# Kernel tuning notes

Measured on AMD Instinct MI355X. Metric: run time of the kernel, lower is better.

## Reference

```python
import jax, jax.numpy as jnp
import numpy as np

DN = ('NCHW', 'OIHW', 'NCHW')

def conv(x, w, b, stride, pad):
    y = jax.lax.conv_general_dilated(x, w, (stride, stride), [(pad, pad), (pad, pad)], dimension_numbers=DN)
    return y if b is None else y + b[None, :, None, None]

def convT(x, w, b, stride, pad):
    # torch ConvTranspose2d weight layout: (in, out, kh, kw)
    wt = jnp.flip(w, (2, 3)).transpose(1, 0, 2, 3)
    p = w.shape[2] - 1 - pad
    y = jax.lax.conv_general_dilated(x, wt, (1, 1), [(p, p), (p, p)], lhs_dilation=(stride, stride), dimension_numbers=DN)
    return y + b[None, :, None, None]

def resblock(x, wa, wb):
    h = conv(jax.nn.relu(x), wa, None, 1, 1)   # 3x3, 128->32, no bias
    h = conv(jax.nn.relu(h), wb, None, 1, 0)   # 1x1, 32->128, no bias
    return x + h

def setup_inputs() -> dict:
    key = jax.random.key(0)
    ks = jax.random.split(key, 32)
    def w(i, shape):
        fan_in = int(np.prod(shape[1:]))
        return jax.random.normal(ks[i], shape, jnp.float32) * (1.0 / np.sqrt(fan_in))
    K, D = 512, 64
    inp = {
        'x':   jax.random.normal(ks[0], (16, 1, 256, 256), jnp.float32),
        'ew1': w(1, (64, 1, 4, 4)),    'eb1': jnp.zeros((64,), jnp.float32),
        'ew2': w(2, (128, 64, 4, 4)),  'eb2': jnp.zeros((128,), jnp.float32),
        'ew3': w(3, (128, 128, 3, 3)), 'eb3': jnp.zeros((128,), jnp.float32),
        'er1a': w(4, (32, 128, 3, 3)), 'er1b': w(5, (128, 32, 1, 1)),
        'er2a': w(6, (32, 128, 3, 3)), 'er2b': w(7, (128, 32, 1, 1)),
        'pw': w(8, (64, 128, 1, 1)),   'pb': jnp.zeros((64,), jnp.float32),
        'codebook': jax.random.uniform(ks[9], (K, D), jnp.float32, -1.0 / K, 1.0 / K),
        'dw1': w(10, (128, 64, 3, 3)), 'db1': jnp.zeros((128,), jnp.float32),
        'dr1a': w(11, (32, 128, 3, 3)), 'dr1b': w(12, (128, 32, 1, 1)),
        'dr2a': w(13, (32, 128, 3, 3)), 'dr2b': w(14, (128, 32, 1, 1)),
        'dtw1': w(15, (128, 64, 4, 4)), 'dtb1': jnp.zeros((64,), jnp.float32),  # ConvT: (in,out,kh,kw)
        'dtw2': w(16, (64, 1, 4, 4)),   'dtb2': jnp.zeros((1,), jnp.float32),
    }
    return inp

def vq(z, codebook, beta=0.25):
    zn = z.transpose(0, 2, 3, 1)                 # NHWC
    flat = zn.reshape(-1, codebook.shape[1])     # [N, D]
    d = jnp.sum(flat * flat, axis=1, keepdims=True) + jnp.sum(codebook * codebook, axis=1) - 2.0 * (flat @ codebook.T)  # [N, K]
    idx = jnp.argmin(d, axis=1)
    enc = jax.nn.one_hot(idx, codebook.shape[0], dtype=z.dtype)  # [N, K]
    q = codebook[idx].reshape(zn.shape)
    e_loss = jnp.mean(jnp.square(jax.lax.stop_gradient(q) - zn))
    q_loss = jnp.mean(jnp.square(q - jax.lax.stop_gradient(zn)))
    loss = q_loss + beta * e_loss
    q_st = zn + jax.lax.stop_gradient(q - zn)    # straight-through
    avg = jnp.mean(enc, axis=0)
    perplexity = jnp.exp(-jnp.sum(avg * jnp.log(avg + 1e-10)))
    return loss, q_st.transpose(0, 3, 1, 2), perplexity, enc

def reference(x, ew1, eb1, ew2, eb2, ew3, eb3, er1a, er1b, er2a, er2b, pw, pb, codebook, dw1, db1, dr1a, dr1b, dr2a, dr2b, dtw1, dtb1, dtw2, dtb2):
    # encoder
    h = jax.nn.relu(conv(x, ew1, eb1, 2, 1))
    h = jax.nn.relu(conv(h, ew2, eb2, 2, 1))
    h = conv(h, ew3, eb3, 1, 1)
    h = resblock(h, er1a, er1b)
    h = resblock(h, er2a, er2b)
    h = jax.nn.relu(h)
    z = conv(h, pw, pb, 1, 0)
    # vector quantizer
    loss, quantized, perplexity, encodings = vq(z, codebook)
    # decoder
    d = conv(quantized, dw1, db1, 1, 1)
    d = resblock(d, dr1a, dr1b)
    d = resblock(d, dr2a, dr2b)
    d = jax.nn.relu(convT(d, dtw1, dtb1, 2, 1))
    x_rec = convT(d, dtw2, dtb2, 2, 1)
    return (loss, x_rec, perplexity, encodings, quantized)
```

## Files before the change

kernel.cpp:

```cpp
#include <hip/hip_runtime.h>

#define TPB 256

typedef __attribute__((ext_vector_type(8))) short s8v;
typedef __attribute__((ext_vector_type(4))) float f4v;
typedef __bf16 bf16x8v __attribute__((ext_vector_type(8)));

__device__ inline short f2b(float f) {
    unsigned u = __builtin_bit_cast(unsigned, f);
    unsigned r = (u + 0x7FFF + ((u >> 16) & 1)) >> 16;
    return (short)r;
}
__device__ inline float b2f(short s) {
    unsigned u = ((unsigned)(unsigned short)s) << 16;
    return __builtin_bit_cast(float, u);
}
__device__ inline f4v mfma16(s8v a, s8v b, f4v c) {
    return __builtin_amdgcn_mfma_f32_16x16x32_bf16(
        __builtin_bit_cast(bf16x8v, a), __builtin_bit_cast(bf16x8v, b), c, 0, 0, 0);
}

struct WtDesc { const float* src; int CO, CI, T, iohw, start; };
struct WtArgs { WtDesc d[13]; int total; };

__global__ __launch_bounds__(256)
void prep_k(WtArgs a, short* dst, const float* __restrict__ cb,
            short* __restrict__ cbh, short* __restrict__ cbl, float* __restrict__ cbsq)
{
    const int bx = blockIdx.x;
    const int tid = threadIdx.x;
    if (bx >= 2560) {
        int c = (bx - 2560) * 256 + tid;
        const float* src = cb + (size_t)c * 64;
        const int nt = c >> 4, rl = c & 15;
        float sq = 0.f;
        for (int d = 0; d < 64; ++d) {
            float v = src[d];
            sq += v * v;
            short h = f2b(v);
            short lo = f2b(v - b2f(h));
            int kc = d >> 5, qd = (d >> 3) & 3, j = d & 7;
            int pos = ((kc * 32 + nt) << 9) + ((qd * 16 + rl) << 3) + j;
            cbh[pos] = h;
            cbl[pos] = lo;
        }
        cbsq[c] = sq;
        return;
    }
    int i = bx * 256 + tid;
    if (i >= a.total) return;
    int s = 0;
    for (int j = 1; j < 13; ++j) if (i >= a.d[j].start) s = j;
    int off = i - a.d[s].start;
    int CI = a.d[s].CI, CO = a.d[s].CO, T = a.d[s].T;
    int KC = CI >> 5, NT = CO >> 4;
    int j    = off & 7;
    int lane = (off >> 3) & 63;
    int rl = lane & 15, qd = lane >> 4;
    int blk = off >> 9;
    int nt  = blk % NT;
    int rest = blk / NT;
    int kc  = rest % KC;
    int tap = rest / KC;
    int co = nt * 16 + rl;
    int ci = kc * 32 + qd * 8 + j;
    float v = a.d[s].iohw ? a.d[s].src[(ci * CO + co) * T + tap]
                          : a.d[s].src[(co * CI + ci) * T + tap];
    dst[i] = f2b(v);
}

__global__ __launch_bounds__(256)
void conv1_k(const float* __restrict__ x, const float* __restrict__ w,
             const float* __restrict__ bias, short* __restrict__ out)
{
    __shared__ float sx[4 * 256];
    const int tid = threadIdx.x;
    const int bx = blockIdx.x;
    const int oh = ((bx & 7) << 4) | (bx >> 3);
    const int n = blockIdx.y;
    const int co = tid & 63, wv = tid >> 6;

    float wr[16];
#pragma unroll
    for (int t = 0; t < 16; ++t) wr[t] = w[co * 16 + t];
    const float b = bias[co];

    const float* xp = x + (size_t)n * 65536;
    for (int e = tid; e < 1024; e += 256) {
        int kh = e >> 8, col = e & 255;
        int ih = oh * 2 - 1 + kh;
        sx[e] = ((unsigned)ih < 256u) ? xp[ih * 256 + col] : 0.f;
    }
    __syncthreads();

    short* op = out + (((size_t)n * 128 + oh) * 128) * 64 + co;
#pragma unroll 4
    for (int i = 0; i < 32; ++i) {
        int ow = wv * 32 + i;
        int iwb = ow * 2 - 1;
        float acc = b;
#pragma unroll
        for (int kh = 0; kh < 4; ++kh) {
#pragma unroll
            for (int kw = 0; kw < 4; ++kw) {
                int iw = iwb + kw;
                float v = ((unsigned)iw < 256u) ? sx[kh * 256 + iw] : 0.f;
                acc = fmaf(v, wr[kh * 4 + kw], acc);
            }
        }
        op[(size_t)ow * 64] = f2b(fmaxf(acc, 0.f));
    }
}

template<int CI, int CO, bool RELU_IN, bool RELU_OUT, bool OUT_F32>
__global__ __launch_bounds__(256)
void pconv3s_k(const short* __restrict__ in, const short* __restrict__ wt,
               const float* __restrict__ bias, void* __restrict__ outv)
{
    constexpr int KC = CI / 32, NT = CO / 16;
    constexpr int NT2 = NT / 2;
    __shared__ short sA[3 * 66 * 40];

    const int tid = threadIdx.x;
    const int bx = blockIdx.x;
    const int oh = ((bx & 7) << 3) | (bx >> 3);
    const int n  = blockIdx.y;
    const short* inb = in + (size_t)n * 4096 * CI;
    const int w = tid >> 6, l = tid & 63, rl = l & 15, qd = l >> 4;
    const int mh = w & 1, nh = w >> 1;

    f4v acc[2][NT2];
#pragma unroll
    for (int a2 = 0; a2 < 2; ++a2)
#pragma unroll
        for (int nt = 0; nt < NT2; ++nt) acc[a2][nt] = (f4v)0.f;

    for (int kc = 0; kc < KC; ++kc) {
        __syncthreads();
        for (int e = tid; e < 792; e += 256) {
            int cell = e >> 2, kcn = e & 3;
            int hr = cell / 66, col = cell - hr * 66;
            int ih = oh - 1 + hr, iw = col - 1;
            s8v v = (s8v)0;
            if ((unsigned)ih < 64u && (unsigned)iw < 64u) {
                v = *(const s8v*)(inb + ((size_t)ih * 64 + iw) * CI + kc * 32 + kcn * 8);
                if (RELU_IN) {
#pragma unroll
                    for (int j = 0; j < 8; ++j) if (v[j] < (short)0) v[j] = 0;
                }
            }
            *(s8v*)&sA[(hr * 66 + col) * 40 + kcn * 8] = v;
        }
        __syncthreads();

#pragma unroll
        for (int tap = 0; tap < 9; ++tap) {
            const int kh = tap / 3, kw = tap % 3;
            s8v af[2];
#pragma unroll
            for (int a2 = 0; a2 < 2; ++a2)
                af[a2] = *(const s8v*)&sA[(kh * 66 + mh * 32 + a2 * 16 + rl + kw) * 40 + qd * 8];
            const short* wb = wt + (((size_t)(tap * KC + kc) * NT + nh * NT2) << 9) + l * 8;
#pragma unroll
            for (int nt = 0; nt < NT2; ++nt) {
                s8v b = *(const s8v*)(wb + ((size_t)nt << 9));
#pragma unroll
                for (int a2 = 0; a2 < 2; ++a2)
                    acc[a2][nt] = mfma16(af[a2], b, acc[a2][nt]);
            }
        }
    }

#pragma unroll
    for (int a2 = 0; a2 < 2; ++a2) {
#pragma unroll
        for (int rg = 0; rg < 4; ++rg) {
            int ow = mh * 32 + a2 * 16 + qd * 4 + rg;
            size_t row = (size_t)n * 4096 + (size_t)oh * 64 + ow;
#pragma unroll
            for (int nt = 0; nt < NT2; ++nt) {
                int co = nh * NT2 * 16 + nt * 16 + rl;
                float v = acc[a2][nt][rg];
                if (bias) v += bias[co];
                if (RELU_OUT) v = fmaxf(v, 0.f);
                if (OUT_F32) ((float*)outv)[row * CO + co] = v;
                else         ((short*)outv)[row * CO + co] = f2b(v);
            }
        }
    }
}

template<int Z>
__global__ __launch_bounds__(256)
void rfuse_k(const short* __restrict__ in, const short* __restrict__ wa,
             const short* __restrict__ wb, short* __restrict__ out,
             const short* __restrict__ wz, const float* __restrict__ zb,
             float* __restrict__ zout)
{
    __shared__ short smem[8704];
    short* sA = smem;
    short* sMid = smem;
    short* sZ = smem;

    const int tid = threadIdx.x;
    const int bx = blockIdx.x;
    const int oh = ((bx & 7) << 3) | (bx >> 3);
    const int n  = blockIdx.y;
    const short* inb = in + (size_t)n * 4096 * 128;
    const int w = tid >> 6, l = tid & 63, rl = l & 15, qd = l >> 4;

    f4v acc1[2];
    acc1[0] = (f4v)0.f; acc1[1] = (f4v)0.f;

    for (int kc = 0; kc < 4; ++kc) {
        __syncthreads();
        for (int e = tid; e < 792; e += 256) {
            int cell = e >> 2, kcn = e & 3;
            int hr = cell / 66, col = cell - hr * 66;
            int ih = oh - 1 + hr, iw = col - 1;
            s8v v = (s8v)0;
            if ((unsigned)ih < 64u && (unsigned)iw < 64u) {
                v = *(const s8v*)(inb + ((size_t)ih * 64 + iw) * 128 + kc * 32 + kcn * 8);
#pragma unroll
                for (int j = 0; j < 8; ++j) if (v[j] < (short)0) v[j] = 0;
            }
            *(s8v*)&sA[(hr * 66 + col) * 40 + kcn * 8] = v;
        }
        __syncthreads();

#pragma unroll
        for (int tap = 0; tap < 9; ++tap) {
            const int kh = tap / 3, kw = tap % 3;
            s8v af = *(const s8v*)&sA[(kh * 66 + w * 16 + rl + kw) * 40 + qd * 8];
            const short* wp = wa + (((size_t)(tap * 4 + kc) * 2) << 9) + l * 8;
            acc1[0] = mfma16(af, *(const s8v*)(wp),       acc1[0]);
            acc1[1] = mfma16(af, *(const s8v*)(wp + 512), acc1[1]);
        }
    }

    __syncthreads();
#pragma unroll
    for (int nt = 0; nt < 2; ++nt)
#pragma unroll
        for (int rg = 0; rg < 4; ++rg) {
            int m  = w * 16 + qd * 4 + rg;
            int co = nt * 16 + rl;
            sMid[m * 40 + co] = f2b(fmaxf(acc1[nt][rg], 0.f));
        }
    __syncthreads();

    f4v acc2[8];
#pragma unroll
    for (int nt = 0; nt < 8; ++nt) acc2[nt] = (f4v)0.f;

    s8v am = *(const s8v*)&sMid[(w * 16 + rl) * 40 + qd * 8];
#pragma unroll
    for (int nt = 0; nt < 8; ++nt) {
        s8v b = *(const s8v*)(wb + ((size_t)nt << 9) + l * 8);
        acc2[nt] = mfma16(am, b, acc2[nt]);
    }

    const size_t sp0 = (size_t)oh * 64;
    if (Z == 0) {
        short* outb = out + (size_t)n * 4096 * 128;
#pragma unroll
        for (int rg = 0; rg < 4; ++rg) {
            int m = w * 16 + qd * 4 + rg;
            size_t sp = sp0 + m;
#pragma unroll
            for (int nt = 0; nt < 8; ++nt) {
                int co = nt * 16 + rl;
                float v = acc2[nt][rg] + b2f(inb[sp * 128 + co]);
                outb[sp * 128 + co] = f2b(v);
            }
        }
    } else {
        __syncthreads();
#pragma unroll
        for (int rg = 0; rg < 4; ++rg) {
            int m = w * 16 + qd * 4 + rg;
            size_t sp = sp0 + m;
#pragma unroll
            for (int nt = 0; nt < 8; ++nt) {
                int co = nt * 16 + rl;
                float v = acc2[nt][rg] + b2f(inb[sp * 128 + co]);
                sZ[m * 136 + co] = f2b(fmaxf(v, 0.f));
            }
        }
        __syncthreads();

        f4v acc3[4];
#pragma unroll
        for (int nt = 0; nt < 4; ++nt) acc3[nt] = (f4v)0.f;
        s8v am2[4];
#pragma unroll
        for (int kc = 0; kc < 4; ++kc)
            am2[kc] = *(const s8v*)&sZ[(w * 16 + rl) * 136 + kc * 32 + qd * 8];
#pragma unroll
        for (int kc = 0; kc < 4; ++kc)
#pragma unroll
            for (int nt = 0; nt < 4; ++nt) {
                s8v b = *(const s8v*)(wz + (((size_t)(kc * 4 + nt)) << 9) + l * 8);
                acc3[nt] = mfma16(am2[kc], b, acc3[nt]);
            }
        const size_t zr0 = (size_t)n * 4096 + (size_t)oh * 64;
#pragma unroll
        for (int rg = 0; rg < 4; ++rg) {
            size_t row = zr0 + w * 16 + qd * 4 + rg;
#pragma unroll
            for (int nt = 0; nt < 4; ++nt) {
                int co = nt * 16 + rl;
                zout[row * 64 + co] = acc3[nt][rg] + zb[co];
            }
        }
    }
}

__global__ __launch_bounds__(256)
void pconv2_k(const short* __restrict__ in, const short* __restrict__ wt,
              const float* __restrict__ bias, short* __restrict__ out)
{
    __shared__ short sA[2 * 4 * 66 * 40];
    const int tid = threadIdx.x;
    const int bx = blockIdx.x;
    const int oh = ((bx & 7) << 3) | (bx >> 3);
    const int n = blockIdx.y;
    const short* inb = in + (size_t)n * 16384 * 64;
    const int w = tid >> 6, l = tid & 63, rl = l & 15, qd = l >> 4;
    const int mh = w & 1, nh = w >> 1;

    f4v acc[2][4];
#pragma unroll
    for (int a2 = 0; a2 < 2; ++a2)
#pragma unroll
        for (int nt = 0; nt < 4; ++nt) acc[a2][nt] = (f4v)0.f;

    for (int kc = 0; kc < 2; ++kc) {
        __syncthreads();
        for (int e = tid; e < 2112; e += 256) {
            int cell = e >> 2, kcn = e & 3;
            int par = cell / 264;
            int rem = cell - par * 264;
            int hr = rem / 66, c = rem - hr * 66;
            int iw = par ? (2 * c - 1) : (2 * c);
            int ih = oh * 2 - 1 + hr;
            s8v v = (s8v)0;
            if ((unsigned)ih < 128u && (unsigned)iw < 128u)
                v = *(const s8v*)(inb + ((size_t)ih * 128 + iw) * 64 + kc * 32 + kcn * 8);
            *(s8v*)&sA[((par * 4 + hr) * 66 + c) * 40 + kcn * 8] = v;
        }
        __syncthreads();

#pragma unroll
        for (int tap = 0; tap < 16; ++tap) {
            const int kh = tap >> 2, kw = tap & 3;
            const int par = 1 - (kw & 1), cofs = kw >> 1;
            s8v af[2];
#pragma unroll
            for (int a2 = 0; a2 < 2; ++a2) {
                int ow = mh * 32 + a2 * 16 + rl;
                af[a2] = *(const s8v*)&sA[((par * 4 + kh) * 66 + ow + cofs) * 40 + qd * 8];
            }
            const short* wb = wt + (((size_t)(tap * 2 + kc) * 8 + nh * 4) << 9) + l * 8;
#pragma unroll
            for (int nt = 0; nt < 4; ++nt) {
                s8v b = *(const s8v*)(wb + ((size_t)nt << 9));
#pragma unroll
                for (int a2 = 0; a2 < 2; ++a2)
                    acc[a2][nt] = mfma16(af[a2], b, acc[a2][nt]);
            }
        }
    }

#pragma unroll
    for (int a2 = 0; a2 < 2; ++a2) {
#pragma unroll
        for (int rg = 0; rg < 4; ++rg) {
            int ow = mh * 32 + a2 * 16 + qd * 4 + rg;
            size_t row = (size_t)n * 4096 + (size_t)oh * 64 + ow;
#pragma unroll
            for (int nt = 0; nt < 4; ++nt) {
                int co = nh * 64 + nt * 16 + rl;
                float v = acc[a2][nt][rg] + bias[co];
                out[row * 128 + co] = f2b(fmaxf(v, 0.f));
            }
        }
    }
}

__global__ __launch_bounds__(256)
void pct1_k(const short* __restrict__ in, const short* __restrict__ wt,
            const float* __restrict__ bias, short* __restrict__ out)
{
    __shared__ short sA[3 * 66 * 40];
    const int tid = threadIdx.x;
    const int bx = blockIdx.x, n = blockIdx.y;
    const int k8 = bx & 7;
    const int P  = (bx >> 3) & 1;
    const int q2 = k8 * 8 + (bx >> 4);
    const int oh0 = (q2 >> 1) * 4 + (q2 & 1);
    const int p = (oh0 + 1) & 1;
    const int ihb0 = (oh0 + 1 - p) >> 1;
    const short* inb = in + (size_t)n * 4096 * 128;
    const int w = tid >> 6, l = tid & 63, rl = l & 15, qd = l >> 4;
    const int mh = w & 1, nh = w >> 1;

    f4v acc[4][2];
#pragma unroll
    for (int a4 = 0; a4 < 4; ++a4)
#pragma unroll
        for (int nt = 0; nt < 2; ++nt) acc[a4][nt] = (f4v)0.f;

    for (int kc = 0; kc < 4; ++kc) {
        __syncthreads();
        for (int e = tid; e < 792; e += 256) {
            int cell = e >> 2, kcn = e & 3;
            int hr = cell / 66, c = cell - hr * 66;
            int ih = ihb0 - 1 + hr, iw = c - 1;
            s8v v = (s8v)0;
            if ((unsigned)ih < 64u && (unsigned)iw < 64u)
                v = *(const s8v*)(inb + ((size_t)ih * 64 + iw) * 128 + kc * 32 + kcn * 8);
            *(s8v*)&sA[(hr * 66 + c) * 40 + kcn * 8] = v;
        }
        __syncthreads();

#pragma unroll
        for (int a = 0; a < 2; ++a)
#pragma unroll
        for (int b = 0; b < 2; ++b) {
            const int kh = p + 2 * a;
            const int kw = (1 - P) + 2 * b;
            const int tap = kh * 4 + kw;
            const int hrw = mh + 1 - a;
            s8v af[4];
#pragma unroll
            for (int a4 = 0; a4 < 4; ++a4)
                af[a4] = *(const s8v*)&sA[(hrw * 66 + a4 * 16 + rl + P - b + 1) * 40 + qd * 8];
            const short* wbp = wt + (((size_t)(tap * 4 + kc) * 4 + nh * 2) << 9) + l * 8;
#pragma unroll
            for (int nt = 0; nt < 2; ++nt) {
                s8v bb = *(const s8v*)(wbp + ((size_t)nt << 9));
#pragma unroll
                for (int a4 = 0; a4 < 4; ++a4)
                    acc[a4][nt] = mfma16(af[a4], bb, acc[a4][nt]);
            }
        }
    }

#pragma unroll
    for (int a4 = 0; a4 < 4; ++a4) {
#pragma unroll
        for (int rg = 0; rg < 4; ++rg) {
            int j = a4 * 16 + qd * 4 + rg;
            int oh = oh0 + 2 * mh, ow = 2 * j + P;
            size_t pb = (((size_t)n * 128 + oh) * 128 + ow) * 64;
#pragma unroll
            for (int nt = 0; nt < 2; ++nt) {
                int co = nh * 32 + nt * 16 + rl;
                float v = acc[a4][nt][rg] + bias[co];
                out[pb + co] = f2b(fmaxf(v, 0.f));
            }
        }
    }
}

__global__ __launch_bounds__(256)
void convt2_k(const short* __restrict__ in, const float* __restrict__ w,
              const float* __restrict__ bias, float* __restrict__ out)
{
    __shared__ float sw[16 * 64];
    const int tid = threadIdx.x;
    for (int e = tid; e < 1024; e += 256) { int ci = e >> 4, tap = e & 15; sw[tap * 64 + ci] = w[e]; }
    __syncthreads();

    const int i = blockIdx.x * 256 + tid;
    const int n = i >> 16, s = i & 65535;
    const int oh = s >> 8, ow = s & 255;

    const int p = (oh + 1) & 1, q = (ow + 1) & 1;
    const int ihb = (oh + 1 - p) >> 1, iwb = (ow + 1 - q) >> 1;

    float acc = bias[0];
#pragma unroll
    for (int a = 0; a < 2; ++a) {
        int ih = ihb - a, kh = p + 2 * a;
        bool vr = (unsigned)ih < 128u;
#pragma unroll
        for (int b = 0; b < 2; ++b) {
            int iw = iwb - b, kw = q + 2 * b;
            if (vr && (unsigned)iw < 128u) {
                const short* ip = in + (((size_t)n * 128 + ih) * 128 + iw) * 64;
                const float* wp = &sw[(kh * 4 + kw) * 64];
#pragma unroll
                for (int c = 0; c < 64; c += 8) {
                    s8v v = *(const s8v*)(ip + c);
#pragma unroll
                    for (int j = 0; j < 8; ++j) acc += b2f(v[j]) * wp[c + j];
                }
            }
        }
    }
    out[i] = acc;
}

__global__ __launch_bounds__(256)
void vqm_k(const float* __restrict__ z, const short* __restrict__ cbh,
           const short* __restrict__ cbl, const float* __restrict__ cbsq,
           const float* __restrict__ cb,
           float* __restrict__ quant, short* __restrict__ qb,
           int* __restrict__ idxp, float* __restrict__ errbuf)
{
    __shared__ float zs[64 * 68];
    __shared__ short scb[2][8192];
    __shared__ int sidx[64];
    __shared__ float serr[4];
    float* qc = (float*)&scb[0][0];

    const int tid = threadIdx.x;
    const int w = tid >> 6, l = tid & 63, rl = l & 15, qd = l >> 4;
    const int r0 = blockIdx.x * 64;

    for (int e = tid; e < 1024; e += 256) {
        int row = e >> 4, c4 = e & 15;
        float4 t = ((const float4*)(z + (size_t)(r0 + row) * 64))[c4];
        *(float4*)&zs[row * 68 + c4 * 4] = t;
    }
    __syncthreads();

    s8v zh[2], zl[2];
#pragma unroll
    for (int kc = 0; kc < 2; ++kc) {
        const float* zp = &zs[(w * 16 + rl) * 68 + kc * 32 + qd * 8];
        s8v hi, lo;
#pragma unroll
        for (int j = 0; j < 8; ++j) {
            float v = zp[j];
            short h = f2b(v);
            hi[j] = h;
            lo[j] = f2b(v - b2f(h));
        }
        zh[kc] = hi; zl[kc] = lo;
    }

    float best[4]; int bidx[4];
#pragma unroll
    for (int rg = 0; rg < 4; ++rg) { best[rg] = 3.4e38f; bidx[rg] = 0; }

    for (int ch = 0; ch < 4; ++ch) {
        __syncthreads();
        for (int e = tid; e < 1024; e += 256) {
            int kcL = e >> 9, rest = e & 511;
            int ntl = rest >> 6, off = rest & 63;
            int srcIdx = (kcL * 32 + ch * 8 + ntl) * 64 + off;
            *(s8v*)&scb[0][e * 8] = ((const s8v*)cbh)[srcIdx];
            *(s8v*)&scb[1][e * 8] = ((const s8v*)cbl)[srcIdx];
        }
        __syncthreads();

        float sq[8];
#pragma unroll
        for (int nt = 0; nt < 8; ++nt) sq[nt] = cbsq[ch * 128 + nt * 16 + rl];

        f4v acc[8];
#pragma unroll
        for (int nt = 0; nt < 8; ++nt) acc[nt] = (f4v)0.f;
#pragma unroll
        for (int kc = 0; kc < 2; ++kc) {
#pragma unroll
            for (int nt = 0; nt < 8; ++nt) {
                s8v bh = *(const s8v*)&scb[0][(kc * 8 + nt) * 512 + l * 8];
                s8v bl = *(const s8v*)&scb[1][(kc * 8 + nt) * 512 + l * 8];
                acc[nt] = mfma16(zh[kc], bh, acc[nt]);
                acc[nt] = mfma16(zh[kc], bl, acc[nt]);
                acc[nt] = mfma16(zl[kc], bh, acc[nt]);
            }
        }

#pragma unroll
        for (int rg = 0; rg < 4; ++rg) {
            float bd = best[rg]; int bi = bidx[rg];
#pragma unroll
            for (int nt = 0; nt < 8; ++nt) {
                float d = sq[nt] - 2.f * acc[nt][rg];
                int code = ch * 128 + nt * 16 + rl;
                if (d < bd) { bd = d; bi = code; }
            }
            best[rg] = bd; bidx[rg] = bi;
        }
    }

#pragma unroll
    for (int rg = 0; rg < 4; ++rg) {
        float bd = best[rg]; int bi = bidx[rg];
#pragma unroll
        for (int off = 1; off < 16; off <<= 1) {
            float od = __shfl_xor(bd, off, 64);
            int   oi = __shfl_xor(bi, off, 64);
            if (od < bd || (od == bd && oi < bi)) { bd = od; bi = oi; }
        }
        if (rl == 0) sidx[w * 16 + qd * 4 + rg] = bi;
    }
    __syncthreads();

    const int n = r0 >> 12, s0 = r0 & 4095;
    float err = 0.f;
#pragma unroll 4
    for (int i = 0; i < 16; ++i) {
        int rr = w * 16 + i;
        int bi = sidx[rr];
        float c = cb[(size_t)bi * 64 + l];
        float zv = zs[rr * 68 + l];
        float dd = zv - c;
        err += dd * dd;
        qb[(size_t)(r0 + rr) * 64 + l] = f2b(c);
        qc[l * 68 + rr] = c;
    }
#pragma unroll
    for (int o = 32; o; o >>= 1) err += __shfl_down(err, o, 64);
    if (l == 0) serr[w] = err;
    if (tid < 64) idxp[r0 + tid] = sidx[tid];
    __syncthreads();

#pragma unroll 4
    for (int dd = 0; dd < 16; ++dd) {
        int d = w * 16 + dd;
        quant[((size_t)(n * 64 + d)) * 4096 + s0 + l] = qc[d * 68 + l];
    }
    if (tid == 0) errbuf[blockIdx.x] = serr[0] + serr[1] + serr[2] + serr[3];
}

__global__ __launch_bounds__(1024)
void fin_k(const int* __restrict__ idxp, const float* __restrict__ errbuf,
           float* out_loss, float* out_perp)
{
    __shared__ int lc[512];
    __shared__ float red[1024];
    const int t = threadIdx.x;
    if (t < 512) lc[t] = 0;
    __syncthreads();
    for (int i = t; i < 65536; i += 1024) atomicAdd(&lc[idxp[i]], 1);
    __syncthreads();
    float v = 0.f;
    if (t < 512) {
        float avg = (float)lc[t] * (1.0f / 65536.0f);
        v = avg * logf(avg + 1e-10f);
    }
    red[t] = v;
    __syncthreads();
    for (int st = 512; st; st >>= 1) { if (t < st) red[t] += red[t + st]; __syncthreads(); }
    if (t == 0) *out_perp = expf(-red[0]);
    __syncthreads();
    red[t] = errbuf[t];
    __syncthreads();
    for (int st = 512; st; st >>= 1) { if (t < st) red[t] += red[t + st]; __syncthreads(); }
    if (t == 0) *out_loss = red[0] * (1.25f / 4194304.0f);
}

__global__ __launch_bounds__(256)
void enc_k(const int* __restrict__ idxp, float4* __restrict__ enc)
{
    int i = blockIdx.x * 256 + threadIdx.x;
    int r = i >> 7, c4 = (i & 127) * 4;
    int k = idxp[r];
    float4 v;
    v.x = (k == c4)     ? 1.f : 0.f;
    v.y = (k == c4 + 1) ? 1.f : 0.f;
    v.z = (k == c4 + 2) ? 1.f : 0.f;
    v.w = (k == c4 + 3) ? 1.f : 0.f;
    enc[i] = v;
}

extern "C" void kernel_launch(void* const* d_in, const int* in_sizes, int n_in,
                              void* d_out, int out_size, void* d_ws, size_t ws_size,
                              hipStream_t stream)
{
    const float* x    = (const float*)d_in[0];
    const float* ew1  = (const float*)d_in[1];
    const float* eb1  = (const float*)d_in[2];
    const float* ew2  = (const float*)d_in[3];
    const float* eb2  = (const float*)d_in[4];
    const float* ew3  = (const float*)d_in[5];
    const float* eb3  = (const float*)d_in[6];
    const float* er1a = (const float*)d_in[7];
    const float* er1b = (const float*)d_in[8];
    const float* er2a = (const float*)d_in[9];
    const float* er2b = (const float*)d_in[10];
    const float* pw   = (const float*)d_in[11];
    const float* pb   = (const float*)d_in[12];
    const float* cb   = (const float*)d_in[13];
    const float* dw1w = (const float*)d_in[14];
    const float* db1  = (const float*)d_in[15];
    const float* dr1a = (const float*)d_in[16];
    const float* dr1b = (const float*)d_in[17];
    const float* dr2a = (const float*)d_in[18];
    const float* dr2b = (const float*)d_in[19];
    const float* dtw1 = (const float*)d_in[20];
    const float* dtb1 = (const float*)d_in[21];
    const float* dtw2 = (const float*)d_in[22];
    const float* dtb2 = (const float*)d_in[23];

    char* wsb = (char*)d_ws;
    short* wbase = (short*)wsb;
    short* wt2   = wbase;
    short* wt3   = wbase + 131072;
    short* wr1a  = wbase + 278528;
    short* wr1b  = wbase + 315392;
    short* wr2a  = wbase + 319488;
    short* wr2b  = wbase + 356352;
    short* wpwt  = wbase + 360448;
    short* wd1   = wbase + 368640;
    short* wdr1a = wbase + 442368;
    short* wdr1b = wbase + 479232;
    short* wdr2a = wbase + 483328;
    short* wdr2b = wbase + 520192;
    short* wtt1  = wbase + 524288;

    short* h2   = (short*)(wsb + 1310720);
    short* buf  = (short*)(wsb + 18087936);
    short* qb   = (short*)(wsb + 39059456);
    float* z    = (float*)(wsb + 47448064);
    int*   idx  = (int*)  (wsb + 64225280);
    if (ws_size < (size_t)64489480) return;

    float* out    = (float*)d_out;
    float* o_loss = out;
    float* xrec   = out + 1;
    float* o_perp = out + 1048577;
    float* enc    = out + 1048578;
    float* quant  = out + 34603010;
    char*  encB = (char*)d_out + (size_t)1048580 * 4;
    short* h1  = (short*)encB;
    short* dt1 = h1 + 16777216;
    short* cbh  = (short*)(encB + ((size_t)120 << 20));
    short* cbl  = cbh + 32768;
    float* cbsq = (float*)(cbl + 32768);
    float* errbuf = (float*)(encB + ((size_t)121 << 20));

    WtArgs wa;
    wa.d[0]  = { ew2,  128,  64, 16, 0, 0      };
    wa.d[1]  = { ew3,  128, 128,  9, 0, 131072 };
    wa.d[2]  = { er1a,  32, 128,  9, 0, 278528 };
    wa.d[3]  = { er1b, 128,  32,  1, 0, 315392 };
    wa.d[4]  = { er2a,  32, 128,  9, 0, 319488 };
    wa.d[5]  = { er2b, 128,  32,  1, 0, 356352 };
    wa.d[6]  = { pw,    64, 128,  1, 0, 360448 };
    wa.d[7]  = { dw1w, 128,  64,  9, 0, 368640 };
    wa.d[8]  = { dr1a,  32, 128,  9, 0, 442368 };
    wa.d[9]  = { dr1b, 128,  32,  1, 0, 479232 };
    wa.d[10] = { dr2a,  32, 128,  9, 0, 483328 };
    wa.d[11] = { dr2b, 128,  32,  1, 0, 520192 };
    wa.d[12] = { dtw1,  64, 128, 16, 1, 524288 };
    wa.total = 655360;
    prep_k<<<dim3(2562), TPB, 0, stream>>>(wa, wbase, cb, cbh, cbl, cbsq);

    conv1_k<<<dim3(128, 16), TPB, 0, stream>>>(x, ew1, eb1, h1);
    pconv2_k<<<dim3(64, 16), TPB, 0, stream>>>(h1, wt2, eb2, h2);
    pconv3s_k<128,128,false,false,false><<<dim3(64,16), TPB, 0, stream>>>(h2, wt3, eb3, buf);
    rfuse_k<0><<<dim3(64,16), TPB, 0, stream>>>(buf, wr1a, wr1b, h2, nullptr, nullptr, nullptr);
    rfuse_k<1><<<dim3(64,16), TPB, 0, stream>>>(h2,  wr2a, wr2b, nullptr, wpwt, pb, z);

    vqm_k<<<dim3(1024), TPB, 0, stream>>>(z, cbh, cbl, cbsq, cb, quant, qb, idx, errbuf);
    fin_k<<<dim3(1), 1024, 0, stream>>>(idx, errbuf, o_loss, o_perp);

    pconv3s_k< 64,128,false,false,false><<<dim3(64,16), TPB, 0, stream>>>(qb, wd1, db1, buf);
    rfuse_k<0><<<dim3(64,16), TPB, 0, stream>>>(buf, wdr1a, wdr1b, h2, nullptr, nullptr, nullptr);
    rfuse_k<0><<<dim3(64,16), TPB, 0, stream>>>(h2,  wdr2a, wdr2b, buf, nullptr, nullptr, nullptr);
    pct1_k<<<dim3(128, 16), TPB, 0, stream>>>(buf, wtt1, dtb1, dt1);
    convt2_k<<<dim3(4096), TPB, 0, stream>>>(dt1, dtw2, dtb2, xrec);

    enc_k<<<dim3(32768), TPB, 0, stream>>>(idx, (float4*)enc);
}
```

Baseline: 551.0 us.

## Merge weight prep with conv1, fold finalize into decoder conv, emit one-hot in VQ

Weight and codebook preparation now run in the same grid as the first encoder conv, which saves one launch and lets the two overlap. The loss and perplexity finalize runs as an extra block inside a specialized decoder 3x3 conv kernel, so fin_k is no longer a separate serial single-block launch. The one-hot encodings are written by the VQ kernel directly from its shared-memory indices, removing the separate enc_k pass that re-read idx. Scratch buffers move from the output region into the workspace, since enc is now written before the decoder finishes, and the workspace requirement grows.

Result: slower. 593.2 us (+7.6%).

```diff
diff --git a/kernel.cpp b/kernel.cpp
--- a/kernel.cpp
+++ b/kernel.cpp
@@ -24,66 +24,67 @@
 struct WtArgs { WtDesc d[13]; int total; };
 
 __global__ __launch_bounds__(256)
-void prep_k(WtArgs a, short* dst, const float* __restrict__ cb,
-            short* __restrict__ cbh, short* __restrict__ cbl, float* __restrict__ cbsq)
-{
-    const int bx = blockIdx.x;
-    const int tid = threadIdx.x;
-    if (bx >= 2560) {
-        int c = (bx - 2560) * 256 + tid;
-        const float* src = cb + (size_t)c * 64;
-        const int nt = c >> 4, rl = c & 15;
-        float sq = 0.f;
-        for (int d = 0; d < 64; ++d) {
-            float v = src[d];
-            sq += v * v;
-            short h = f2b(v);
-            short lo = f2b(v - b2f(h));
-            int kc = d >> 5, qd = (d >> 3) & 3, j = d & 7;
-            int pos = ((kc * 32 + nt) << 9) + ((qd * 16 + rl) << 3) + j;
-            cbh[pos] = h;
-            cbl[pos] = lo;
-        }
-        cbsq[c] = sq;
-        return;
-    }
-    int i = bx * 256 + tid;
-    if (i >= a.total) return;
-    int s = 0;
-    for (int j = 1; j < 13; ++j) if (i >= a.d[j].start) s = j;
-    int off = i - a.d[s].start;
-    int CI = a.d[s].CI, CO = a.d[s].CO, T = a.d[s].T;
-    int KC = CI >> 5, NT = CO >> 4;
-    int j    = off & 7;
-    int lane = (off >> 3) & 63;
-    int rl = lane & 15, qd = lane >> 4;
-    int blk = off >> 9;
-    int nt  = blk % NT;
-    int rest = blk / NT;
-    int kc  = rest % KC;
-    int tap = rest / KC;
-    int co = nt * 16 + rl;
-    int ci = kc * 32 + qd * 8 + j;
-    float v = a.d[s].iohw ? a.d[s].src[(ci * CO + co) * T + tap]
-                          : a.d[s].src[(co * CI + ci) * T + tap];
-    dst[i] = f2b(v);
-}
-
-__global__ __launch_bounds__(256)
-void conv1_k(const float* __restrict__ x, const float* __restrict__ w,
-             const float* __restrict__ bias, short* __restrict__ out)
+void head_k(WtArgs a, short* dst, const float* __restrict__ cb,
+            short* __restrict__ cbh, short* __restrict__ cbl, float* __restrict__ cbsq,
+            const float* __restrict__ x, const float* __restrict__ ew1,
+            const float* __restrict__ eb1, short* __restrict__ h1)
 {
     __shared__ float sx[4 * 256];
+    const int gbx = blockIdx.x;
     const int tid = threadIdx.x;
-    const int bx = blockIdx.x;
-    const int oh = ((bx & 7) << 4) | (bx >> 3);
-    const int n = blockIdx.y;
+
+    if (gbx >= 2048) {
+        const int pbx = gbx - 2048;
+        if (pbx >= 2560) {
+            int c = (pbx - 2560) * 256 + tid;
+            const float* src = cb + (size_t)c * 64;
+            const int nt = c >> 4, rl = c & 15;
+            float sq = 0.f;
+            for (int d = 0; d < 64; ++d) {
+                float v = src[d];
+                sq += v * v;
+                short h = f2b(v);
+                short lo = f2b(v - b2f(h));
+                int kc = d >> 5, qd = (d >> 3) & 3, j = d & 7;
+                int pos = ((kc * 32 + nt) << 9) + ((qd * 16 + rl) << 3) + j;
+                cbh[pos] = h;
+                cbl[pos] = lo;
+            }
+            cbsq[c] = sq;
+            return;
+        }
+        int i = pbx * 256 + tid;
+        if (i >= a.total) return;
+        int s = 0;
+        for (int j = 1; j < 13; ++j) if (i >= a.d[j].start) s = j;
+        int off = i - a.d[s].start;
+        int CI = a.d[s].CI, CO = a.d[s].CO, T = a.d[s].T;
+        int KC = CI >> 5, NT = CO >> 4;
+        int j    = off & 7;
+        int lane = (off >> 3) & 63;
+        int rl = lane & 15, qd = lane >> 4;
+        int blk = off >> 9;
+        int nt  = blk % NT;
+        int rest = blk / NT;
+        int kc  = rest % KC;
+        int tap = rest / KC;
+        int co = nt * 16 + rl;
+        int ci = kc * 32 + qd * 8 + j;
+        float v = a.d[s].iohw ? a.d[s].src[(ci * CO + co) * T + tap]
+                              : a.d[s].src[(co * CI + ci) * T + tap];
+        dst[i] = f2b(v);
+        return;
+    }
+
+    const int n = gbx >> 7;
+    const int bxl = gbx & 127;
+    const int oh = ((bxl & 7) << 4) | (bxl >> 3);
     const int co = tid & 63, wv = tid >> 6;
 
     float wr[16];
 #pragma unroll
-    for (int t = 0; t < 16; ++t) wr[t] = w[co * 16 + t];
-    const float b = bias[co];
+    for (int t = 0; t < 16; ++t) wr[t] = ew1[co * 16 + t];
+    const float b = eb1[co];
 
     const float* xp = x + (size_t)n * 65536;
     for (int e = tid; e < 1024; e += 256) {
@@ -93,7 +94,7 @@
     }
     __syncthreads();
 
-    short* op = out + (((size_t)n * 128 + oh) * 128) * 64 + co;
+    short* op = h1 + (((size_t)n * 128 + oh) * 128) * 64 + co;
 #pragma unroll 4
     for (int i = 0; i < 32; ++i) {
         int ow = wv * 32 + i;
@@ -185,6 +186,102 @@
                 if (RELU_OUT) v = fmaxf(v, 0.f);
                 if (OUT_F32) ((float*)outv)[row * CO + co] = v;
                 else         ((short*)outv)[row * CO + co] = f2b(v);
+            }
+        }
+    }
+}
+
+__global__ __launch_bounds__(256)
+void dec1_k(const short* __restrict__ in, const short* __restrict__ wt,
+            const float* __restrict__ bias, short* __restrict__ out,
+            const int* __restrict__ idxp, const float* __restrict__ errbuf,
+            float* __restrict__ o_loss, float* __restrict__ o_perp)
+{
+    __shared__ short sA[3 * 66 * 40];
+    __shared__ int lc[512];
+    __shared__ float red2[256];
+
+    const int gbx = blockIdx.x;
+    const int tid = threadIdx.x;
+
+    if (gbx >= 1024) {
+        lc[tid] = 0; lc[tid + 256] = 0;
+        __syncthreads();
+        for (int i = tid; i < 65536; i += 256) atomicAdd(&lc[idxp[i]], 1);
+        __syncthreads();
+        float a1 = (float)lc[tid] * (1.0f / 65536.0f);
+        float a2 = (float)lc[tid + 256] * (1.0f / 65536.0f);
+        float v = a1 * logf(a1 + 1e-10f) + a2 * logf(a2 + 1e-10f);
+        red2[tid] = v;
+        __syncthreads();
+        for (int st = 128; st; st >>= 1) { if (tid < st) red2[tid] += red2[tid + st]; __syncthreads(); }
+        if (tid == 0) *o_perp = expf(-red2[0]);
+        __syncthreads();
+        float e = 0.f;
+        for (int i = tid; i < 1024; i += 256) e += errbuf[i];
+        red2[tid] = e;
+        __syncthreads();
+        for (int st = 128; st; st >>= 1) { if (tid < st) red2[tid] += red2[tid + st]; __syncthreads(); }
+        if (tid == 0) *o_loss = red2[0] * (1.25f / 4194304.0f);
+        return;
+    }
+
+    constexpr int CI = 64, NT2 = 4;
+    const int bxl = gbx & 63;
+    const int oh = ((bxl & 7) << 3) | (bxl >> 3);
+    const int n  = gbx >> 6;
+    const short* inb = in + (size_t)n * 4096 * CI;
+    const int w = tid >> 6, l = tid & 63, rl = l & 15, qd = l >> 4;
+    const int mh = w & 1, nh = w >> 1;
+
+    f4v acc[2][NT2];
+#pragma unroll
+    for (int a2 = 0; a2 < 2; ++a2)
+#pragma unroll
+        for (int nt = 0; nt < NT2; ++nt) acc[a2][nt] = (f4v)0.f;
+
+    for (int kc = 0; kc < 2; ++kc) {
+        __syncthreads();
+        for (int e = tid; e < 792; e += 256) {
+            int cell = e >> 2, kcn = e & 3;
+            int hr = cell / 66, col = cell - hr * 66;
+            int ih = oh - 1 + hr, iw = col - 1;
+            s8v v = (s8v)0;
+            if ((unsigned)ih < 64u && (unsigned)iw < 64u)
+                v = *(const s8v*)(inb + ((size_t)ih * 64 + iw) * CI + kc * 32 + kcn * 8);
+            *(s8v*)&sA[(hr * 66 + col) * 40 + kcn * 8] = v;
+        }
+        __syncthreads();
+
+#pragma unroll
+        for (int tap = 0; tap < 9; ++tap) {
+            const int kh = tap / 3, kw = tap % 3;
+            s8v af[2];
+#pragma unroll
+            for (int a2 = 0; a2 < 2; ++a2)
+                af[a2] = *(const s8v*)&sA[(kh * 66 + mh * 32 + a2 * 16 + rl + kw) * 40 + qd * 8];
+            const short* wb = wt + (((size_t)(tap * 2 + kc) * 8 + nh * NT2) << 9) + l * 8;
+#pragma unroll
+            for (int nt = 0; nt < NT2; ++nt) {
+                s8v b = *(const s8v*)(wb + ((size_t)nt << 9));
+#pragma unroll
+                for (int a2 = 0; a2 < 2; ++a2)
+                    acc[a2][nt] = mfma16(af[a2], b, acc[a2][nt]);
+            }
+        }
+    }
+
+#pragma unroll
+    for (int a2 = 0; a2 < 2; ++a2) {
+#pragma unroll
+        for (int rg = 0; rg < 4; ++rg) {
+            int ow = mh * 32 + a2 * 16 + qd * 4 + rg;
+            size_t row = (size_t)n * 4096 + (size_t)oh * 64 + ow;
+#pragma unroll
+            for (int nt = 0; nt < NT2; ++nt) {
+                int co = nh * NT2 * 16 + nt * 16 + rl;
+                float v = acc[a2][nt][rg] + bias[co];
+                out[row * 128 + co] = f2b(v);
             }
         }
     }
@@ -508,7 +605,8 @@
            const short* __restrict__ cbl, const float* __restrict__ cbsq,
            const float* __restrict__ cb,
            float* __restrict__ quant, short* __restrict__ qb,
-           int* __restrict__ idxp, float* __restrict__ errbuf)
+           int* __restrict__ idxp, float* __restrict__ errbuf,
+           float4* __restrict__ enc)
 {
     __shared__ float zs[64 * 68];
     __shared__ short scb[2][8192];
@@ -627,47 +725,17 @@
         quant[((size_t)(n * 64 + d)) * 4096 + s0 + l] = qc[d * 68 + l];
     }
     if (tid == 0) errbuf[blockIdx.x] = serr[0] + serr[1] + serr[2] + serr[3];
-}
-
-__global__ __launch_bounds__(1024)
-void fin_k(const int* __restrict__ idxp, const float* __restrict__ errbuf,
-           float* out_loss, float* out_perp)
-{
-    __shared__ int lc[512];
-    __shared__ float red[1024];
-    const int t = threadIdx.x;
-    if (t < 512) lc[t] = 0;
-    __syncthreads();
-    for (int i = t; i < 65536; i += 1024) atomicAdd(&lc[idxp[i]], 1);
-    __syncthreads();
-    float v = 0.f;
-    if (t < 512) {
-        float avg = (float)lc[t] * (1.0f / 65536.0f);
-        v = avg * logf(avg + 1e-10f);
-    }
-    red[t] = v;
-    __syncthreads();
-    for (int st = 512; st; st >>= 1) { if (t < st) red[t] += red[t + st]; __syncthreads(); }
-    if (t == 0) *out_perp = expf(-red[0]);
-    __syncthreads();
-    red[t] = errbuf[t];
-    __syncthreads();
-    for (int st = 512; st; st >>= 1) { if (t < st) red[t] += red[t + st]; __syncthreads(); }
-    if (t == 0) *out_loss = red[0] * (1.25f / 4194304.0f);
-}
-
-__global__ __launch_bounds__(256)
-void enc_k(const int* __restrict__ idxp, float4* __restrict__ enc)
-{
-    int i = blockIdx.x * 256 + threadIdx.x;
-    int r = i >> 7, c4 = (i & 127) * 4;
-    int k = idxp[r];
-    float4 v;
-    v.x = (k == c4)     ? 1.f : 0.f;
-    v.y = (k == c4 + 1) ? 1.f : 0.f;
-    v.z = (k == c4 + 2) ? 1.f : 0.f;
-    v.w = (k == c4 + 3) ? 1.f : 0.f;
-    enc[i] = v;
+
+    for (int e = tid; e < 8192; e += 256) {
+        int row = e >> 7, c4 = (e & 127) * 4;
+        int k = sidx[row];
+        float4 v;
+        v.x = (k == c4)     ? 1.f : 0.f;
+        v.y = (k == c4 + 1) ? 1.f : 0.f;
+        v.z = (k == c4 + 2) ? 1.f : 0.f;
+        v.w = (k == c4 + 3) ? 1.f : 0.f;
+        enc[(size_t)(r0 + row) * 128 + (e & 127)] = v;
+    }
 }
 
 extern "C" void kernel_launch(void* const* d_in, const int* in_sizes, int n_in,
@@ -719,8 +787,13 @@
     short* buf  = (short*)(wsb + 18087936);
     short* qb   = (short*)(wsb + 39059456);
     float* z    = (float*)(wsb + 47448064);
-    int*   idx  = (int*)  (wsb + 64225280);
-    if (ws_size < (size_t)64489480) return;
+    short* dt1  = (short*)(wsb + 47448064);
+    int*   idx  = (int*)  (wsb + 81002496);
+    short* cbh  = (short*)(wsb + 81264640);
+    short* cbl  = (short*)(wsb + 81330176);
+    float* cbsq = (float*)(wsb + 81395712);
+    float* errbuf = (float*)(wsb + 81397760);
+    if (ws_size < (size_t)81401856) return;
 
     float* out    = (float*)d_out;
     float* o_loss = out;
@@ -728,13 +801,7 @@
     float* o_perp = out + 1048577;
     float* enc    = out + 1048578;
     float* quant  = out + 34603010;
-    char*  encB = (char*)d_out + (size_t)1048580 * 4;
-    short* h1  = (short*)encB;
-    short* dt1 = h1 + 16777216;
-    short* cbh  = (short*)(encB + ((size_t)120 << 20));
-    short* cbl  = cbh + 32768;
-    float* cbsq = (float*)(cbl + 32768);
-    float* errbuf = (float*)(encB + ((size_t)121 << 20));
+    short* h1 = (short*)((char*)d_out + (size_t)1048580 * 4);
 
     WtArgs wa;
     wa.d[0]  = { ew2,  128,  64, 16, 0, 0      };
@@ -751,22 +818,19 @@
     wa.d[11] = { dr2b, 128,  32,  1, 0, 520192 };
     wa.d[12] = { dtw1,  64, 128, 16, 1, 524288 };
     wa.total = 655360;
-    prep_k<<<dim3(2562), TPB, 0, stream>>>(wa, wbase, cb, cbh, cbl, cbsq);
-
-    conv1_k<<<dim3(128, 16), TPB, 0, stream>>>(x, ew1, eb1, h1);
+
+    head_k<<<dim3(4610), TPB, 0, stream>>>(wa, wbase, cb, cbh, cbl, cbsq, x, ew1, eb1, h1);
+
     pconv2_k<<<dim3(64, 16), TPB, 0, stream>>>(h1, wt2, eb2, h2);
     pconv3s_k<128,128,false,false,false><<<dim3(64,16), TPB, 0, stream>>>(h2, wt3, eb3, buf);
     rfuse_k<0><<<dim3(64,16), TPB, 0, stream>>>(buf, wr1a, wr1b, h2, nullptr, nullptr, nullptr);
     rfuse_k<1><<<dim3(64,16), TPB, 0, stream>>>(h2,  wr2a, wr2b, nullptr, wpwt, pb, z);
 
-    vqm_k<<<dim3(1024), TPB, 0, stream>>>(z, cbh, cbl, cbsq, cb, quant, qb, idx, errbuf);
-    fin_k<<<dim3(1), 1024, 0, stream>>>(idx, errbuf, o_loss, o_perp);
-
-    pconv3s_k< 64,128,false,false,false><<<dim3(64,16), TPB, 0, stream>>>(qb, wd1, db1, buf);
+    vqm_k<<<dim3(1024), TPB, 0, stream>>>(z, cbh, cbl, cbsq, cb, quant, qb, idx, errbuf, (float4*)enc);
+
+    dec1_k<<<dim3(1025), TPB, 0, stream>>>(qb, wd1, db1, buf, idx, errbuf, o_loss, o_perp);
     rfuse_k<0><<<dim3(64,16), TPB, 0, stream>>>(buf, wdr1a, wdr1b, h2, nullptr, nullptr, nullptr);
     rfuse_k<0><<<dim3(64,16), TPB, 0, stream>>>(h2,  wdr2a, wdr2b, buf, nullptr, nullptr, nullptr);
     pct1_k<<<dim3(128, 16), TPB, 0, stream>>>(buf, wtt1, dtb1, dt1);
     convt2_k<<<dim3(4096), TPB, 0, stream>>>(dt1, dtw2, dtb2, xrec);
-
-    enc_k<<<dim3(32768), TPB, 0, stream>>>(idx, (float4*)enc);
-}
+}
```
